# Performance work log

Hardware: AMD Instinct MI355X
Metric: run time of the kernel (lower is better)

The kernel has to match this reference:

```python
import jax, jax.numpy as jnp
import numpy as np

L, B, IN, H, OUT = 4, 4096, 1024, 1024, 1024


def setup_inputs() -> dict:
    key = jax.random.key(0)
    ks = jax.random.split(key, 9)
    std = 1.0 / (H + IN) ** 0.5
    return {
        "x": jax.random.normal(ks[0], (B, IN), jnp.float32),
        "h_prev": jax.random.normal(ks[1], (L, B, H), jnp.float32),
        "c_prev": jax.random.normal(ks[2], (L, B, H), jnp.float32),
        "Wi": jax.random.uniform(ks[3], (L, IN, 4 * H), jnp.float32, -std, std),
        "Wh": jax.random.uniform(ks[4], (L, H, 4 * H), jnp.float32, -std, std),
        "bi": jax.random.uniform(ks[5], (L, 4 * H), jnp.float32, -std, std),
        "bh": jax.random.uniform(ks[6], (L, 4 * H), jnp.float32, -std, std),
        "fc_W": jax.random.uniform(ks[7], (H, OUT), jnp.float32, -std, std),
        "fc_b": jax.random.uniform(ks[8], (OUT,), jnp.float32, -std, std),
    }


def _lstm_cell(x, h, c, Wi, Wh, bi, bh):
    # gates: [B, 4H], split into (input, forget, cell, output)
    gates = x @ Wi + bi + h @ Wh + bh
    i, f, g, o = jnp.split(gates, 4, axis=1)
    i, f, o = jax.nn.sigmoid(i), jax.nn.sigmoid(f), jax.nn.sigmoid(o)
    g = jnp.tanh(g)
    c_cur = f * c + i * g
    h_cur = o * jnp.tanh(c_cur)
    return h_cur, c_cur


def reference(x, h_prev, c_prev, Wi, Wh, bi, bh, fc_W, fc_b):
    h_out, c_out = [], []
    x_in = x
    for l in range(L):  # fixed small layer loop
        h_cur, c_cur = _lstm_cell(x_in, h_prev[l], c_prev[l], Wi[l], Wh[l], bi[l], bh[l])
        h_out.append(h_cur)
        c_out.append(c_cur)
        x_in = h_cur
    h_out = jnp.stack(h_out, axis=0)
    c_out = jnp.stack(c_out, axis=0)
    y = h_out[-1] @ fc_W + fc_b
    return y, h_out, c_out
```

## Files before the change

kernel.cpp:

```cpp
#include <hip/hip_runtime.h>

#define B_    4096
#define H_    1024
#define NLAY  4

typedef __attribute__((ext_vector_type(8))) short bf16x8;
typedef __attribute__((ext_vector_type(4))) short s16x4;
typedef __attribute__((ext_vector_type(4))) float f32x4;
typedef unsigned short ushort_t;

__device__ __forceinline__ ushort_t f2bf(float f) {
  unsigned u = __builtin_bit_cast(unsigned, f);
  u += 0x7FFFu + ((u >> 16) & 1u);
  return (ushort_t)(u >> 16);
}

__device__ __forceinline__ float fast_sigmoid(float x) {
  float e = __expf(-fabsf(x));
  float s = 1.0f / (1.0f + e);
  return x >= 0.0f ? s : 1.0f - s;
}
__device__ __forceinline__ float fast_tanh(float x) {
  float e = __expf(-2.0f * fabsf(x));
  float t = (1.0f - e) / (1.0f + e);
  return x >= 0.0f ? t : -t;
}

#define GLDS16(gsrc, ldst)                                                  \
  __builtin_amdgcn_global_load_lds(                                         \
      (__attribute__((address_space(1))) void*)(gsrc),                      \
      (__attribute__((address_space(3))) void*)(ldst), 16, 0, 0)

#define BAR()                                                               \
  { asm volatile("" ::: "memory");                                          \
    __builtin_amdgcn_s_barrier();                                           \
    asm volatile("" ::: "memory"); }

#define WAITV(N)                                                            \
  { asm volatile("s_waitcnt vmcnt(" #N ")" ::: "memory");                   \
    __builtin_amdgcn_sched_barrier(0); }

#define LGKM0()                                                             \
  { asm volatile("s_waitcnt lgkmcnt(0)" ::: "memory");                      \
    __builtin_amdgcn_sched_barrier(0); }

__device__ __forceinline__ bf16x8 dsr128(unsigned addr, int imm) {
  bf16x8 r;
  asm volatile("ds_read_b128 %0, %1 offset:%c2"
               : "=v"(r)
               : "v"(addr), "i"(imm));
  return r;
}

__global__ __launch_bounds__(512, 1) void lstm8(
    const ushort_t* __restrict__ aX, const ushort_t* __restrict__ aH,
    const float* __restrict__ cprev, const float* __restrict__ bi,
    const float* __restrict__ bh, const ushort_t* __restrict__ wtl,
    float* __restrict__ hout, float* __restrict__ cout,
    ushort_t* __restrict__ hbfout) {
  __shared__ __align__(16) char sL[131072];

  const int tid  = threadIdx.x;
  const int lane = tid & 63;
  const int wid  = tid >> 6;
  const int wm   = wid >> 2;
  const int wn   = wid & 3;
  const int bid  = (blockIdx.x & 7) * 32 + (blockIdx.x >> 3);
  const int bm   = bid & 15;
  const int bn   = bid >> 4;

  const int fr = lane & 15;
  const int oF = lane >> 4;
  const int sw = (oF ^ ((fr >> 1) & 3)) * 16;

  const unsigned sBase = (unsigned)(size_t)&sL[0];
  const unsigned aAddr = sBase + (unsigned)(wm * 16384 + fr * 64 + sw);
  const unsigned bAddr = sBase + (unsigned)(65536 + (wn >> 1) * 16384 +
                                            (wn & 1) * 4096 + fr * 64 + sw);

  const int oA = (tid & 3) ^ ((tid >> 3) & 3);
  const size_t aOff0 = (size_t)(bm * 256 + (tid >> 2)) * 1024 + oA * 8;
  const size_t aOff1 = aOff0 + (size_t)128 * 1024;
  const ushort_t* wtBn = wtl + (size_t)bn * 524288;

  f32x4 acc[8][4];
#pragma unroll
  for (int m = 0; m < 8; ++m)
#pragma unroll
    for (int g = 0; g < 4; ++g) acc[m][g] = (f32x4){0.f, 0.f, 0.f, 0.f};

  bf16x8 ar[4][2], br0[2][2], br1[2][2];

#define STAGE_A(PAR, HALF, TT)                                               \
  {                                                                          \
    const ushort_t* s0 =                                                     \
        (((TT) < 16) ? aX : aH) + ((HALF) ? aOff1 : aOff0) + ((TT) & 15) * 64; \
    char* d = sL + (PAR) * 32768 + (HALF) * 16384 + wid * 1024;              \
    GLDS16(s0, d);                                                           \
    GLDS16(s0 + 32, d + 8192);                                               \
  }
#define STAGE_B(PAR, HALF, TT)                                               \
  {                                                                          \
    const ushort_t* s0 =                                                     \
        wtBn + (size_t)((TT) & 31) * 16384 + (HALF) * 8192 + tid * 8;        \
    char* d = sL + 65536 + (PAR) * 32768 + (HALF) * 16384 + wid * 1024;      \
    GLDS16(s0, d);                                                           \
    GLDS16(s0 + 4096, d + 8192);                                             \
  }
#define RD_A(PAR, MH)                                                        \
  _Pragma("unroll") for (int mp = 0; mp < 4; ++mp)                           \
      _Pragma("unroll") for (int kh = 0; kh < 2; ++kh)                       \
      ar[mp][kh] = dsr128(aAddr, (PAR) * 32768 + kh * 8192 +                 \
                                     ((MH) * 4 + mp) * 1024);
#define RD_B(PAR, NH, BR)                                                    \
  _Pragma("unroll") for (int gg = 0; gg < 2; ++gg)                           \
      _Pragma("unroll") for (int kh = 0; kh < 2; ++kh)                       \
      BR[gg][kh] = dsr128(bAddr, (PAR) * 32768 + kh * 8192 +                 \
                                     ((NH) * 2 + gg) * 1024);
#define MM(MH, NH, BR)                                                       \
  __builtin_amdgcn_s_setprio(1);                                             \
  _Pragma("unroll") for (int gg = 0; gg < 2; ++gg)                           \
      _Pragma("unroll") for (int mp = 0; mp < 4; ++mp)                       \
      _Pragma("unroll") for (int kh = 0; kh < 2; ++kh)                       \
      acc[(MH) * 4 + mp][(NH) * 2 + gg] =                                    \
          __builtin_amdgcn_mfma_f32_16x16x32_bf16(                           \
              ar[mp][kh], BR[gg][kh], acc[(MH) * 4 + mp][(NH) * 2 + gg],     \
              0, 0, 0);                                                      \
  __builtin_amdgcn_s_setprio(0);

  STAGE_A(0, 0, 0)
  STAGE_A(0, 1, 0)
  STAGE_B(0, 0, 0)
  STAGE_B(0, 1, 0)
  STAGE_B(1, 0, 1)
  STAGE_B(1, 1, 1)
  WAITV(4)
  BAR()

#pragma unroll 1
  for (int t2 = 0; t2 < 32; t2 += 2) {
    RD_A(0, 0) RD_B(0, 0, br0)
    STAGE_A(1, 0, t2 + 1)
    BAR()
    LGKM0()
    MM(0, 0, br0)
    BAR()

    RD_B(0, 1, br1)
    STAGE_A(1, 1, t2 + 1)
    BAR()
    LGKM0()
    MM(0, 1, br1)
    BAR()

    RD_A(0, 1)
    STAGE_B(0, 0, (t2 + 2))
    BAR()
    LGKM0()
    MM(1, 0, br0)
    BAR()

    STAGE_B(0, 1, (t2 + 2))
    BAR()
    MM(1, 1, br1)
    WAITV(4)
    BAR()

    RD_A(1, 0) RD_B(1, 0, br0)
    STAGE_A(0, 0, (t2 + 2))
    BAR()
    LGKM0()
    MM(0, 0, br0)
    BAR()

    RD_B(1, 1, br1)
    STAGE_A(0, 1, (t2 + 2))
    BAR()
    LGKM0()
    MM(0, 1, br1)
    BAR()

    RD_A(1, 1)
    STAGE_B(1, 0, (t2 + 3))
    BAR()
    LGKM0()
    MM(1, 0, br0)
    BAR()

    STAGE_B(1, 1, (t2 + 3))
    BAR()
    MM(1, 1, br1)
    WAITV(4)
    BAR()
  }
#undef STAGE_A
#undef STAGE_B
#undef RD_A
#undef RD_B
#undef MM

  WAITV(0)
  __syncthreads();

  const int hcolL = wn * 16 + fr;
  const int hcol  = bn * 64 + hcolL;
  float bsum[4];
#pragma unroll
  for (int g = 0; g < 4; ++g)
    bsum[g] = bi[g * 1024 + hcol] + bh[g * 1024 + hcol];

#define LSTRIDE 68
  float* LF = (float*)sL;
  const int crow = tid >> 4;
  const int cc4  = (tid & 15) * 4;
  {
    const float* cp0 = cprev + (size_t)(bm * 256) * 1024 + bn * 64;
#pragma unroll
    for (int i = 0; i < 8; ++i) {
      const int row = i * 32 + crow;
      f32x4 v = *(const f32x4*)(cp0 + (size_t)row * 1024 + cc4);
      *(f32x4*)(LF + row * LSTRIDE + cc4) = v;
    }
  }
  __syncthreads();
  float cv[8][4], hv[8][4];
#pragma unroll
  for (int m = 0; m < 8; ++m) {
    const int rowb = wm * 128 + m * 16 + oF * 4;
#pragma unroll
    for (int r = 0; r < 4; ++r) {
      const float cp = LF[(rowb + r) * LSTRIDE + hcolL];
      const float gi = fast_sigmoid(acc[m][0][r] + bsum[0]);
      const float gf = fast_sigmoid(acc[m][1][r] + bsum[1]);
      const float gg = fast_tanh(acc[m][2][r] + bsum[2]);
      const float go = fast_sigmoid(acc[m][3][r] + bsum[3]);
      const float c  = gf * cp + gi * gg;
      cv[m][r] = c;
      hv[m][r] = go * fast_tanh(c);
    }
  }
  __syncthreads();
#pragma unroll
  for (int m = 0; m < 8; ++m) {
    const int rowb = wm * 128 + m * 16 + oF * 4;
#pragma unroll
    for (int r = 0; r < 4; ++r) LF[(rowb + r) * LSTRIDE + hcolL] = cv[m][r];
  }
  __syncthreads();
  {
    float* co0 = cout + (size_t)(bm * 256) * 1024 + bn * 64;
#pragma unroll
    for (int i = 0; i < 8; ++i) {
      const int row = i * 32 + crow;
      f32x4 v = *(const f32x4*)(LF + row * LSTRIDE + cc4);
      *(f32x4*)(co0 + (size_t)row * 1024 + cc4) = v;
    }
  }
  __syncthreads();
#pragma unroll
  for (int m = 0; m < 8; ++m) {
    const int rowb = wm * 128 + m * 16 + oF * 4;
#pragma unroll
    for (int r = 0; r < 4; ++r) LF[(rowb + r) * LSTRIDE + hcolL] = hv[m][r];
  }
  __syncthreads();
  {
    float* ho0 = hout + (size_t)(bm * 256) * 1024 + bn * 64;
    ushort_t* hb0 = hbfout + (size_t)(bm * 256) * 1024 + bn * 64;
#pragma unroll
    for (int i = 0; i < 8; ++i) {
      const int row = i * 32 + crow;
      f32x4 v = *(const f32x4*)(LF + row * LSTRIDE + cc4);
      *(f32x4*)(ho0 + (size_t)row * 1024 + cc4) = v;
      s16x4 hb;
#pragma unroll
      for (int j = 0; j < 4; ++j) hb[j] = (short)f2bf(v[j]);
      *(s16x4*)(hb0 + (size_t)row * 1024 + cc4) = hb;
    }
  }
#undef LSTRIDE
}

__global__ __launch_bounds__(512) void packW(const float* __restrict__ Wi,
                                             const float* __restrict__ Wh,
                                             ushort_t* __restrict__ wt) {
  __shared__ ushort_t t16[64 * 256];
  const int bn = blockIdx.x;
  const int T  = blockIdx.y;
  const int l  = blockIdx.z;
  const int tid = threadIdx.x;
  const int kq = tid >> 6, cc = tid & 63;
  const int k0 = T * 64;
  const float* W = (k0 < 1024)
                       ? (Wi + (size_t)l * 1024 * 4096 + (size_t)k0 * 4096)
                       : (Wh + (size_t)l * 1024 * 4096 + (size_t)(k0 - 1024) * 4096);
#pragma unroll
  for (int kk = 0; kk < 8; ++kk) {
    const int kl = kq * 8 + kk;
#pragma unroll
    for (int g = 0; g < 4; ++g) {
      const float v = W[(size_t)kl * 4096 + g * 1024 + bn * 64 + cc];
      const int p = (cc >> 4) * 64 + g * 16 + (cc & 15);
      t16[kl * 256 + p] = f2bf(v);
    }
  }
  __syncthreads();
#pragma unroll
  for (int half = 0; half < 2; ++half) {
    ushort_t* img =
        wt + (((size_t)l * 16 + bn) * 32 + T) * 16384 + half * 8192;
#pragma unroll
    for (int c = 0; c < 2; ++c) {
      const int idx = c * 512 + tid;
      const int kh = idx >> 9;
      const int r  = (idx >> 2) & 127;
      const int s  = idx & 3;
      const int o  = s ^ ((r >> 1) & 3);
      const int klb = kh * 32 + o * 8;
      const int pg  = half * 128 + r;
      bf16x8 ov;
#pragma unroll
      for (int j = 0; j < 8; ++j) ov[j] = (short)t16[(klb + j) * 256 + pg];
      *(bf16x8*)(img + (size_t)idx * 8) = ov;
    }
  }
}

__device__ __forceinline__ int swz(int row, int kelem) {
  return ((row * 64 + kelem) * 2) ^ ((row & 7) << 4);
}

__global__ __launch_bounds__(512) void fc_kernel(
    const ushort_t* __restrict__ wtfc, const ushort_t* __restrict__ abf,
    const float* __restrict__ bias, float* __restrict__ y) {
  __shared__ __align__(16) char sA[128 * 64 * 2];
  __shared__ __align__(16) char sB[64 * 64 * 2];
  const int tid  = threadIdx.x;
  const int lane = tid & 63;
  const int wid  = tid >> 6;
  const int wm   = wid >> 2;
  const int wn   = wid & 3;
  const int bid  = (blockIdx.x & 7) * 64 + (blockIdx.x >> 3);
  const int bm   = bid & 31;
  const int bn   = bid >> 5;

  f32x4 acc[4];
#pragma unroll
  for (int m = 0; m < 4; ++m) acc[m] = (f32x4){0.f, 0.f, 0.f, 0.f};

  const int rloc = wid * 8 + (lane >> 3);
  const int jA   = (lane & 7) ^ ((lane >> 3) & 7);
  const ushort_t* aSrc = abf + (size_t)(bm * 128 + rloc) * 1024 + jA * 8;

  for (int ks = 0; ks < 16; ++ks) {
    __syncthreads();
    GLDS16(wtfc + (size_t)(bn * 16 + ks) * 4096 + tid * 8, sB + wid * 1024);
    const int off = ks * 64;
    GLDS16(aSrc + off,             sA + wid * 1024);
    GLDS16(aSrc + off + 64 * 1024, sA + 8192 + wid * 1024);
    __syncthreads();
#pragma unroll
    for (int kk = 0; kk < 64; kk += 32) {
      const int ke = kk + (lane >> 4) * 8;
      bf16x8 a[4];
#pragma unroll
      for (int m = 0; m < 4; ++m)
        a[m] = *(const bf16x8*)(sA + swz(wm * 64 + m * 16 + (lane & 15), ke));
      bf16x8 b = *(const bf16x8*)(sB + swz(wn * 16 + (lane & 15), ke));
#pragma unroll
      for (int m = 0; m < 4; ++m)
        acc[m] = __builtin_amdgcn_mfma_f32_16x16x32_bf16(a[m], b, acc[m], 0, 0, 0);
    }
  }
  const int col = bn * 64 + wn * 16 + (lane & 15);
  const float bb = bias[col];
#pragma unroll
  for (int m = 0; m < 4; ++m) {
    const int row0 = bm * 128 + wm * 64 + m * 16 + ((lane >> 4) << 2);
#pragma unroll
    for (int r = 0; r < 4; ++r)
      y[(size_t)(row0 + r) * 1024 + col] = acc[m][r] + bb;
  }
}

__global__ __launch_bounds__(512) void transposeFc(const float* __restrict__ W,
                                                   ushort_t* __restrict__ wt) {
  const int bn = blockIdx.x;
  const int ks = blockIdx.y;
  const int tid = threadIdx.x;
  const int c  = tid & 63;
  const int ko = (tid >> 6) * 8;
  float v[8];
#pragma unroll
  for (int j = 0; j < 8; ++j)
    v[j] = W[(size_t)(ks * 64 + ko + j) * 1024 + bn * 64 + c];
  bf16x8 o;
#pragma unroll
  for (int j = 0; j < 8; ++j) o[j] = (short)f2bf(v[j]);
  ushort_t* tile = wt + ((size_t)bn * 16 + ks) * 4096;
  *(bf16x8*)((char*)tile + swz(c, ko)) = o;
}

__global__ __launch_bounds__(256) void cvt_bf16(const float* __restrict__ s,
                                                ushort_t* __restrict__ d,
                                                int n8) {
  const int i = blockIdx.x * 256 + threadIdx.x;
  if (i >= n8) return;
  const float* p = s + (size_t)i * 8;
  f32x4 a = ((const f32x4*)p)[0];
  f32x4 b = ((const f32x4*)p)[1];
  bf16x8 o;
#pragma unroll
  for (int j = 0; j < 4; ++j) {
    o[j]     = (short)f2bf(a[j]);
    o[4 + j] = (short)f2bf(b[j]);
  }
  *(bf16x8*)(d + (size_t)i * 8) = o;
}

extern "C" void kernel_launch(void* const* d_in, const int* in_sizes, int n_in,
                              void* d_out, int out_size, void* d_ws,
                              size_t ws_size, hipStream_t stream) {
  const float* x     = (const float*)d_in[0];
  const float* hprev = (const float*)d_in[1];
  const float* cprev = (const float*)d_in[2];
  const float* Wi    = (const float*)d_in[3];
  const float* Wh    = (const float*)d_in[4];
  const float* bi    = (const float*)d_in[5];
  const float* bh    = (const float*)d_in[6];
  const float* fcW   = (const float*)d_in[7];
  const float* fcb   = (const float*)d_in[8];

  float* out = (float*)d_out;
  const size_t BH = (size_t)B_ * H_;
  float* y    = out;
  float* hout = out + BH;
  float* cout = out + 5 * BH;

  const size_t WT_ELEMS = (size_t)4 * 16 * 32 * 16384;
  const size_t FC_ELEMS = (size_t)16 * 16 * 4096;
  ushort_t* wt      = (ushort_t*)d_ws;
  ushort_t* fcwt    = wt + WT_ELEMS;
  ushort_t* xbf     = fcwt + FC_ELEMS;
  ushort_t* hprevbf = xbf + BH;
  ushort_t* houtbf  = hprevbf + 4 * BH;

  packW<<<dim3(16, 32, 4), dim3(512), 0, stream>>>(Wi, Wh, wt);
  transposeFc<<<dim3(16, 16), dim3(512), 0, stream>>>(fcW, fcwt);
  cvt_bf16<<<dim3((int)(BH / 8 / 256)), dim3(256), 0, stream>>>(x, xbf,
                                                                (int)(BH / 8));
  cvt_bf16<<<dim3((int)(4 * BH / 8 / 256)), dim3(256), 0, stream>>>(
      hprev, hprevbf, (int)(4 * BH / 8));

  for (int l = 0; l < NLAY; ++l) {
    const ushort_t* aX  = (l == 0) ? xbf : (houtbf + (size_t)(l - 1) * BH);
    const ushort_t* wtl = wt + (size_t)l * 16 * 32 * 16384;
    lstm8<<<dim3(256), dim3(512), 0, stream>>>(
        aX, hprevbf + (size_t)l * BH, cprev + (size_t)l * BH, bi + l * 4096,
        bh + l * 4096, wtl, hout + (size_t)l * BH, cout + (size_t)l * BH,
        houtbf + (size_t)l * BH);
  }
  fc_kernel<<<dim3(512), dim3(512), 0, stream>>>(fcwt, houtbf + 3 * BH, fcb, y);
}
```

Baseline: 384.5 us.

## Halve LSTM GEMM waves to 4 with 128x128 per-wave tiles and regrouped block mapping

```diff
diff --git a/kernel.cpp b/kernel.cpp
--- a/kernel.cpp
+++ b/kernel.cpp
@@ -52,7 +52,7 @@
   return r;
 }
 
-__global__ __launch_bounds__(512, 1) void lstm8(
+__global__ __launch_bounds__(256, 1) void lstm8(
     const ushort_t* __restrict__ aX, const ushort_t* __restrict__ aH,
     const float* __restrict__ cprev, const float* __restrict__ bi,
     const float* __restrict__ bh, const ushort_t* __restrict__ wtl,
@@ -63,11 +63,11 @@
   const int tid  = threadIdx.x;
   const int lane = tid & 63;
   const int wid  = tid >> 6;
-  const int wm   = wid >> 2;
-  const int wn   = wid & 3;
-  const int bid  = (blockIdx.x & 7) * 32 + (blockIdx.x >> 3);
-  const int bm   = bid & 15;
-  const int bn   = bid >> 4;
+  const int wm   = wid >> 1;
+  const int wn   = wid & 1;
+  const int xcd = blockIdx.x & 7, bj = blockIdx.x >> 3;
+  const int bm  = (xcd >> 2) * 8 + (bj >> 2);
+  const int bn  = (xcd & 3) * 4 + (bj & 3);
 
   const int fr = lane & 15;
   const int oF = lane >> 4;
@@ -75,37 +75,47 @@
 
   const unsigned sBase = (unsigned)(size_t)&sL[0];
   const unsigned aAddr = sBase + (unsigned)(wm * 16384 + fr * 64 + sw);
-  const unsigned bAddr = sBase + (unsigned)(65536 + (wn >> 1) * 16384 +
-                                            (wn & 1) * 4096 + fr * 64 + sw);
-
-  const int oA = (tid & 3) ^ ((tid >> 3) & 3);
-  const size_t aOff0 = (size_t)(bm * 256 + (tid >> 2)) * 1024 + oA * 8;
-  const size_t aOff1 = aOff0 + (size_t)128 * 1024;
+  const unsigned bAddr = sBase + (unsigned)(65536 + wn * 16384 + fr * 64 + sw);
+
+  int aof[4];
+#pragma unroll
+  for (int c = 0; c < 4; ++c) {
+    const int q = tid + c * 256;
+    const int kh = q >> 9, r = (q >> 2) & 127, s = q & 3;
+    const int o = s ^ ((r >> 1) & 3);
+    aof[c] = r * 1024 + kh * 32 + o * 8;
+  }
+  const int aof0 = aof[0], aof1 = aof[1], aof2 = aof[2], aof3 = aof[3];
+  const size_t aRowBase = (size_t)(bm * 256) * 1024;
   const ushort_t* wtBn = wtl + (size_t)bn * 524288;
 
-  f32x4 acc[8][4];
+  f32x4 acc[8][8];
 #pragma unroll
   for (int m = 0; m < 8; ++m)
 #pragma unroll
-    for (int g = 0; g < 4; ++g) acc[m][g] = (f32x4){0.f, 0.f, 0.f, 0.f};
-
-  bf16x8 ar[4][2], br0[2][2], br1[2][2];
+    for (int n = 0; n < 8; ++n) acc[m][n] = (f32x4){0.f, 0.f, 0.f, 0.f};
+
+  bf16x8 ar[4][2], br0[4][2], br1[4][2];
 
 #define STAGE_A(PAR, HALF, TT)                                               \
   {                                                                          \
-    const ushort_t* s0 =                                                     \
-        (((TT) < 16) ? aX : aH) + ((HALF) ? aOff1 : aOff0) + ((TT) & 15) * 64; \
+    const ushort_t* bp = (((TT) < 16) ? aX : aH) + aRowBase +                \
+                         (HALF) * 131072 + ((TT) & 15) * 64;                 \
     char* d = sL + (PAR) * 32768 + (HALF) * 16384 + wid * 1024;              \
-    GLDS16(s0, d);                                                           \
-    GLDS16(s0 + 32, d + 8192);                                               \
+    GLDS16(bp + aof0, d);                                                    \
+    GLDS16(bp + aof1, d + 4096);                                             \
+    GLDS16(bp + aof2, d + 8192);                                             \
+    GLDS16(bp + aof3, d + 12288);                                            \
   }
 #define STAGE_B(PAR, HALF, TT)                                               \
   {                                                                          \
-    const ushort_t* s0 =                                                     \
-        wtBn + (size_t)((TT) & 31) * 16384 + (HALF) * 8192 + tid * 8;        \
+    const ushort_t* bp =                                                     \
+        wtBn + (size_t)(TT) * 16384 + (HALF) * 8192 + tid * 8;               \
     char* d = sL + 65536 + (PAR) * 32768 + (HALF) * 16384 + wid * 1024;      \
-    GLDS16(s0, d);                                                           \
-    GLDS16(s0 + 4096, d + 8192);                                             \
+    GLDS16(bp, d);                                                           \
+    GLDS16(bp + 2048, d + 4096);                                             \
+    GLDS16(bp + 4096, d + 8192);                                             \
+    GLDS16(bp + 6144, d + 12288);                                            \
   }
 #define RD_A(PAR, MH)                                                        \
   _Pragma("unroll") for (int mp = 0; mp < 4; ++mp)                           \
@@ -113,20 +123,18 @@
       ar[mp][kh] = dsr128(aAddr, (PAR) * 32768 + kh * 8192 +                 \
                                      ((MH) * 4 + mp) * 1024);
 #define RD_B(PAR, NH, BR)                                                    \
-  _Pragma("unroll") for (int gg = 0; gg < 2; ++gg)                           \
+  _Pragma("unroll") for (int gg = 0; gg < 4; ++gg)                           \
       _Pragma("unroll") for (int kh = 0; kh < 2; ++kh)                       \
       BR[gg][kh] = dsr128(bAddr, (PAR) * 32768 + kh * 8192 +                 \
-                                     ((NH) * 2 + gg) * 1024);
+                                     ((NH) * 4 + gg) * 1024);
 #define MM(MH, NH, BR)                                                       \
-  __builtin_amdgcn_s_setprio(1);                                             \
-  _Pragma("unroll") for (int gg = 0; gg < 2; ++gg)                           \
+  _Pragma("unroll") for (int gg = 0; gg < 4; ++gg)                           \
       _Pragma("unroll") for (int mp = 0; mp < 4; ++mp)                       \
       _Pragma("unroll") for (int kh = 0; kh < 2; ++kh)                       \
-      acc[(MH) * 4 + mp][(NH) * 2 + gg] =                                    \
+      acc[(MH) * 4 + mp][(NH) * 4 + gg] =                                    \
           __builtin_amdgcn_mfma_f32_16x16x32_bf16(                           \
-              ar[mp][kh], BR[gg][kh], acc[(MH) * 4 + mp][(NH) * 2 + gg],     \
-              0, 0, 0);                                                      \
-  __builtin_amdgcn_s_setprio(0);
+              ar[mp][kh], BR[gg][kh], acc[(MH) * 4 + mp][(NH) * 4 + gg],     \
+              0, 0, 0);
 
   STAGE_A(0, 0, 0)
   STAGE_A(0, 1, 0)
@@ -134,7 +142,7 @@
   STAGE_B(0, 1, 0)
   STAGE_B(1, 0, 1)
   STAGE_B(1, 1, 1)
-  WAITV(4)
+  WAITV(8)
   BAR()
 
 #pragma unroll 1
@@ -154,43 +162,43 @@
     BAR()
 
     RD_A(0, 1)
-    STAGE_B(0, 0, (t2 + 2))
+    STAGE_B(0, 0, t2 + 2)
     BAR()
     LGKM0()
     MM(1, 0, br0)
     BAR()
 
-    STAGE_B(0, 1, (t2 + 2))
+    STAGE_B(0, 1, t2 + 2)
     BAR()
     MM(1, 1, br1)
-    WAITV(4)
+    WAITV(8)
     BAR()
 
     RD_A(1, 0) RD_B(1, 0, br0)
-    STAGE_A(0, 0, (t2 + 2))
+    STAGE_A(0, 0, t2 + 2)
     BAR()
     LGKM0()
     MM(0, 0, br0)
     BAR()
 
     RD_B(1, 1, br1)
-    STAGE_A(0, 1, (t2 + 2))
+    STAGE_A(0, 1, t2 + 2)
     BAR()
     LGKM0()
     MM(0, 1, br1)
     BAR()
 
     RD_A(1, 1)
-    STAGE_B(1, 0, (t2 + 3))
+    STAGE_B(1, 0, t2 + 3)
     BAR()
     LGKM0()
     MM(1, 0, br0)
     BAR()
 
-    STAGE_B(1, 1, (t2 + 3))
+    STAGE_B(1, 1, t2 + 3)
     BAR()
     MM(1, 1, br1)
-    WAITV(4)
+    WAITV(8)
     BAR()
   }
 #undef STAGE_A
@@ -202,12 +210,14 @@
   WAITV(0)
   __syncthreads();
 
-  const int hcolL = wn * 16 + fr;
-  const int hcol  = bn * 64 + hcolL;
-  float bsum[4];
-#pragma unroll
-  for (int g = 0; g < 4; ++g)
-    bsum[g] = bi[g * 1024 + hcol] + bh[g * 1024 + hcol];
+  float bsum[2][4];
+#pragma unroll
+  for (int hg = 0; hg < 2; ++hg)
+#pragma unroll
+    for (int g = 0; g < 4; ++g) {
+      const int col = g * 1024 + bn * 64 + wn * 32 + hg * 16 + fr;
+      bsum[hg][g] = bi[col] + bh[col];
+    }
 
 #define LSTRIDE 68
   float* LF = (float*)sL;
@@ -216,27 +226,41 @@
   {
     const float* cp0 = cprev + (size_t)(bm * 256) * 1024 + bn * 64;
 #pragma unroll
-    for (int i = 0; i < 8; ++i) {
-      const int row = i * 32 + crow;
+    for (int i = 0; i < 16; ++i) {
+      const int row = i * 16 + crow;
       f32x4 v = *(const f32x4*)(cp0 + (size_t)row * 1024 + cc4);
       *(f32x4*)(LF + row * LSTRIDE + cc4) = v;
     }
   }
   __syncthreads();
-  float cv[8][4], hv[8][4];
+  float hv[8][2][4];
 #pragma unroll
   for (int m = 0; m < 8; ++m) {
     const int rowb = wm * 128 + m * 16 + oF * 4;
 #pragma unroll
-    for (int r = 0; r < 4; ++r) {
-      const float cp = LF[(rowb + r) * LSTRIDE + hcolL];
-      const float gi = fast_sigmoid(acc[m][0][r] + bsum[0]);
-      const float gf = fast_sigmoid(acc[m][1][r] + bsum[1]);
-      const float gg = fast_tanh(acc[m][2][r] + bsum[2]);
-      const float go = fast_sigmoid(acc[m][3][r] + bsum[3]);
-      const float c  = gf * cp + gi * gg;
-      cv[m][r] = c;
-      hv[m][r] = go * fast_tanh(c);
+    for (int hg = 0; hg < 2; ++hg) {
+      const int hc = wn * 32 + hg * 16 + fr;
+#pragma unroll
+      for (int r = 0; r < 4; ++r) {
+        const float cp = LF[(rowb + r) * LSTRIDE + hc];
+        const float gi = fast_sigmoid(acc[m][0 + hg][r] + bsum[hg][0]);
+        const float gf = fast_sigmoid(acc[m][2 + hg][r] + bsum[hg][1]);
+        const float gg = fast_tanh(acc[m][4 + hg][r] + bsum[hg][2]);
+        const float go = fast_sigmoid(acc[m][6 + hg][r] + bsum[hg][3]);
+        const float c  = gf * cp + gi * gg;
+        LF[(rowb + r) * LSTRIDE + hc] = c;
+        hv[m][hg][r] = go * fast_tanh(c);
+      }
+    }
+  }
+  __syncthreads();
+  {
+    float* co0 = cout + (size_t)(bm * 256) * 1024 + bn * 64;
+#pragma unroll
+    for (int i = 0; i < 16; ++i) {
+      const int row = i * 16 + crow;
+      f32x4 v = *(const f32x4*)(LF + row * LSTRIDE + cc4);
+      *(f32x4*)(co0 + (size_t)row * 1024 + cc4) = v;
     }
   }
   __syncthreads();
@@ -244,32 +268,19 @@
   for (int m = 0; m < 8; ++m) {
     const int rowb = wm * 128 + m * 16 + oF * 4;
 #pragma unroll
-    for (int r = 0; r < 4; ++r) LF[(rowb + r) * LSTRIDE + hcolL] = cv[m][r];
-  }
-  __syncthreads();
-  {
-    float* co0 = cout + (size_t)(bm * 256) * 1024 + bn * 64;
-#pragma unroll
-    for (int i = 0; i < 8; ++i) {
-      const int row = i * 32 + crow;
-      f32x4 v = *(const f32x4*)(LF + row * LSTRIDE + cc4);
-      *(f32x4*)(co0 + (size_t)row * 1024 + cc4) = v;
-    }
-  }
-  __syncthreads();
-#pragma unroll
-  for (int m = 0; m < 8; ++m) {
-    const int rowb = wm * 128 + m * 16 + oF * 4;
-#pragma unroll
-    for (int r = 0; r < 4; ++r) LF[(rowb + r) * LSTRIDE + hcolL] = hv[m][r];
+    for (int hg = 0; hg < 2; ++hg) {
+      const int hc = wn * 32 + hg * 16 + fr;
+#pragma unroll
+      for (int r = 0; r < 4; ++r) LF[(rowb + r) * LSTRIDE + hc] = hv[m][hg][r];
+    }
   }
   __syncthreads();
   {
     float* ho0 = hout + (size_t)(bm * 256) * 1024 + bn * 64;
     ushort_t* hb0 = hbfout + (size_t)(bm * 256) * 1024 + bn * 64;
 #pragma unroll
-    for (int i = 0; i < 8; ++i) {
-      const int row = i * 32 + crow;
+    for (int i = 0; i < 16; ++i) {
+      const int row = i * 16 + crow;
       f32x4 v = *(const f32x4*)(LF + row * LSTRIDE + cc4);
       *(f32x4*)(ho0 + (size_t)row * 1024 + cc4) = v;
       s16x4 hb;
@@ -300,29 +311,26 @@
 #pragma unroll
     for (int g = 0; g < 4; ++g) {
       const float v = W[(size_t)kl * 4096 + g * 1024 + bn * 64 + cc];
-      const int p = (cc >> 4) * 64 + g * 16 + (cc & 15);
+      const int p = (cc >> 5) * 128 + g * 32 + ((cc >> 4) & 1) * 16 + (cc & 15);
       t16[kl * 256 + p] = f2bf(v);
     }
   }
   __syncthreads();
-#pragma unroll
-  for (int half = 0; half < 2; ++half) {
-    ushort_t* img =
-        wt + (((size_t)l * 16 + bn) * 32 + T) * 16384 + half * 8192;
-#pragma unroll
-    for (int c = 0; c < 2; ++c) {
-      const int idx = c * 512 + tid;
-      const int kh = idx >> 9;
-      const int r  = (idx >> 2) & 127;
-      const int s  = idx & 3;
-      const int o  = s ^ ((r >> 1) & 3);
-      const int klb = kh * 32 + o * 8;
-      const int pg  = half * 128 + r;
-      bf16x8 ov;
-#pragma unroll
-      for (int j = 0; j < 8; ++j) ov[j] = (short)t16[(klb + j) * 256 + pg];
-      *(bf16x8*)(img + (size_t)idx * 8) = ov;
-    }
+  ushort_t* tile = wt + (((size_t)l * 16 + bn) * 32 + T) * 16384;
+#pragma unroll
+  for (int c = 0; c < 4; ++c) {
+    const int idx = c * 512 + tid;
+    const int half = idx >> 10;
+    const int kh = (idx >> 9) & 1;
+    const int r  = (idx >> 2) & 127;
+    const int s  = idx & 3;
+    const int o  = s ^ ((r >> 1) & 3);
+    const int klb = kh * 32 + o * 8;
+    const int p   = half * 128 + r;
+    bf16x8 ov;
+#pragma unroll
+    for (int j = 0; j < 8; ++j) ov[j] = (short)t16[(klb + j) * 256 + p];
+    *(bf16x8*)(tile + (size_t)idx * 8) = ov;
   }
 }
 
@@ -455,7 +463,7 @@
   for (int l = 0; l < NLAY; ++l) {
     const ushort_t* aX  = (l == 0) ? xbf : (houtbf + (size_t)(l - 1) * BH);
     const ushort_t* wtl = wt + (size_t)l * 16 * 32 * 16384;
-    lstm8<<<dim3(256), dim3(512), 0, stream>>>(
+    lstm8<<<dim3(256), dim3(256), 0, stream>>>(
         aX, hprevbf + (size_t)l * BH, cprev + (size_t)l * BH, bi + l * 4096,
         bh + l * 4096, wtl, hout + (size_t)l * BH, cout + (size_t)l * BH,
         houtbf + (size_t)l * BH);
```

After: 446.3 us. +16.1%, slower.
